# Kernel optimization log

Hardware: AMD Instinct MI355X
Metric: run time of the kernel (lower is better)

The kernel has to match this reference:

```python
import jax, jax.numpy as jnp
import numpy as np

N_CH = 256          # EEG channels = graph nodes
T = 100000          # timesteps
CNN_OUT = 32
GRU_H = 64
GNN_H = 32
N_CLS = 2
THRESH = 0.7


def _conv1d(x, w, b, stride, pad):
    # x: [N, C_in, L], w: [C_out, C_in, K]
    y = jax.lax.conv_general_dilated(
        x, w, window_strides=(stride,), padding=[(pad, pad)],
        dimension_numbers=("NCH", "OIH", "NCH"))
    return y + b[None, :, None]


def _gru_last_hidden(xs, wih, whh, bih, bhh):
    # xs: [S, N, in], returns final hidden [N, H] (PyTorch GRU equations)
    H = whh.shape[1]
    h0 = jnp.zeros((xs.shape[1], H), xs.dtype)

    def step(h, x):
        gi = x @ wih.T + bih          # [N, 3H]
        gh = h @ whh.T + bhh
        i_r, i_z, i_n = jnp.split(gi, 3, axis=-1)
        h_r, h_z, h_n = jnp.split(gh, 3, axis=-1)
        r = jax.nn.sigmoid(i_r + h_r)
        z = jax.nn.sigmoid(i_z + h_z)
        n = jnp.tanh(i_n + r * h_n)
        h = (1.0 - z) * n + z * h
        return h, None

    hT, _ = jax.lax.scan(step, h0, xs)
    return hT


def _pairwise_corrcoef(x):
    x = x - x.mean(axis=1, keepdims=True)
    x = x / (x.std(axis=1, keepdims=True, ddof=1) + 1e-6)  # torch std is unbiased
    return (x @ x.T) / x.shape[1]


def _gcn(x, A_hat, w, b):
    # PyG GCNConv: A_hat @ (x @ W^T) + b  (sym-normalized adj w/ self-loops)
    return A_hat @ (x @ w.T) + b


def setup_inputs() -> dict:
    key = jax.random.key(0)
    ks = jax.random.split(key, 24)
    r = lambda i, shape, s: (jax.random.normal(ks[i], shape, jnp.float32) * s)
    d = {
        "data": r(0, (N_CH, T), 1.0),
        "conv1_w": r(1, (8, 1, 11), 0.3), "conv1_b": r(2, (8,), 0.1),
        "conv2_w": r(3, (16, 8, 7), 0.1), "conv2_b": r(4, (16,), 0.1),
        "conv3_w": r(5, (CNN_OUT, 16, 5), 0.1), "conv3_b": r(6, (CNN_OUT,), 0.1),
        "gru_wih_f": r(7, (3 * GRU_H, CNN_OUT), 0.1), "gru_whh_f": r(8, (3 * GRU_H, GRU_H), 0.1),
        "gru_bih_f": r(9, (3 * GRU_H,), 0.05), "gru_bhh_f": r(10, (3 * GRU_H,), 0.05),
        "gru_wih_b": r(11, (3 * GRU_H, CNN_OUT), 0.1), "gru_whh_b": r(12, (3 * GRU_H, GRU_H), 0.1),
        "gru_bih_b": r(13, (3 * GRU_H,), 0.05), "gru_bhh_b": r(14, (3 * GRU_H,), 0.05),
        "gcn1_w": r(15, (GNN_H, 2 * GRU_H), 0.1), "gcn1_b": r(16, (GNN_H,), 0.05),
        "gcn2_w": r(17, (GNN_H, GNN_H), 0.15), "gcn2_b": r(18, (GNN_H,), 0.05),
        "cls_w": r(19, (N_CLS, GNN_H), 0.15), "cls_b": r(20, (N_CLS,), 0.05),
    }
    return d


def reference(data, conv1_w, conv1_b, conv2_w, conv2_b, conv3_w, conv3_b,
              gru_wih_f, gru_whh_f, gru_bih_f, gru_bhh_f,
              gru_wih_b, gru_whh_b, gru_bih_b, gru_bhh_b,
              gcn1_w, gcn1_b, gcn2_w, gcn2_b, cls_w, cls_b):
    x = data[:, None, :]                                 # [N, 1, T]
    x = jax.nn.relu(_conv1d(x, conv1_w, conv1_b, 5, 5))  # [N, 8, 20000]
    x = jax.nn.relu(_conv1d(x, conv2_w, conv2_b, 5, 3))  # [N, 16, 4000]
    x = jax.nn.relu(_conv1d(x, conv3_w, conv3_b, 5, 2))  # [N, 32, 800]
    xs = jnp.transpose(x, (2, 0, 1))                     # [S=800, N, 32]

    h_f = _gru_last_hidden(xs, gru_wih_f, gru_whh_f, gru_bih_f, gru_bhh_f)
    h_b = _gru_last_hidden(xs[::-1], gru_wih_b, gru_whh_b, gru_bih_b, gru_bhh_b)
    # torch h_n.permute(1,0,2).reshape(N,-1) -> concat [fwd, bwd]
    h_n = jnp.concatenate([h_f, h_b], axis=-1)           # [N, 128]

    corr = _pairwise_corrcoef(h_n)                       # [N, N]
    # dense adjacency = thresholded |corr|; diagonal is ~1 so self-loops present
    # (matches PyG add_remaining_self_loops: already there). Always nonempty.
    A = (jnp.abs(corr) > THRESH).astype(h_n.dtype)
    deg = A.sum(axis=1)
    dinv = jax.lax.rsqrt(jnp.maximum(deg, 1e-12))
    A_hat = A * dinv[:, None] * dinv[None, :]            # D^-1/2 A D^-1/2

    h = jax.nn.relu(_gcn(h_n, A_hat, gcn1_w, gcn1_b))
    h = jax.nn.relu(_gcn(h, A_hat, gcn2_w, gcn2_b))
    graph_emb = h.mean(axis=0, keepdims=True)            # [1, GNN_H]
    return graph_emb @ cls_w.T + cls_b                   # [1, N_CLS]
```

## Files before the change

### kernel.cpp

```cpp
#include <hip/hip_runtime.h>
#include <math.h>

#define N_CH 256
#define T_IN 100000
#define L1O 20000
#define L2O 4000
#define L3O 800
#define C1 8
#define C2 16
#define C3 32

#define TILE3 25
#define NY2   125
#define NY1   627
#define ND    3141

__device__ __forceinline__ float sigm(float x) {
    x = fminf(fmaxf(x, -30.0f), 30.0f);
    return 1.0f / (1.0f + __expf(-x));
}
__device__ __forceinline__ float tanhfast(float x) {
    x = fminf(fmaxf(x, -15.0f), 15.0f);
    float e = __expf(-2.0f * x);
    return (1.0f - e) / (1.0f + e);
}
__device__ __forceinline__ float bcast(float v, int lane) {
    return __int_as_float(__builtin_amdgcn_readlane(__float_as_int(v), lane));
}
__device__ __forceinline__ float f4e(const float4& v, int e) {
    return ((const float*)&v)[e];
}

__global__ __launch_bounds__(256) void k_conv(
    const float* __restrict__ data,
    const float* __restrict__ w1, const float* __restrict__ b1,
    const float* __restrict__ w2, const float* __restrict__ b2,
    const float* __restrict__ w3, const float* __restrict__ b3,
    float* __restrict__ x3)
{
    __shared__ __align__(16) float sd[ND];
    __shared__ __align__(16) float sy1[NY1][C1];
    __shared__ __align__(16) float sy2[NY2][C2];

    const int tid = threadIdx.x;
    const int tb  = blockIdx.x;
    const int ch  = blockIdx.y;
    const int t0    = tb * TILE3;
    const int dbase = 3125 * tb - 70;
    const int ubase = 625 * tb - 13;
    const int sbase = 125 * tb - 2;

    const float* dch = data + (size_t)ch * T_IN;
    for (int e = tid; e < ND; e += 256) {
        int g = dbase + e;
        sd[e] = (g >= 0 && g < T_IN) ? dch[g] : 0.0f;
    }
    __syncthreads();

    for (int u = tid; u < NY1; u += 256) {
        int ug = ubase + u;
        bool ok = (ug >= 0 && ug < L1O);
        float t[11];
        #pragma unroll
        for (int k = 0; k < 11; ++k) t[k] = sd[5 * u + k];
        float acc[8];
        #pragma unroll
        for (int c = 0; c < 8; ++c) acc[c] = b1[c];
        #pragma unroll
        for (int k = 0; k < 11; ++k) {
            float tv = t[k];
            #pragma unroll
            for (int c = 0; c < 8; ++c) acc[c] = fmaf(w1[c * 11 + k], tv, acc[c]);
        }
        float4 o0, o1;
        o0.x = ok ? fmaxf(acc[0], 0.f) : 0.f;  o0.y = ok ? fmaxf(acc[1], 0.f) : 0.f;
        o0.z = ok ? fmaxf(acc[2], 0.f) : 0.f;  o0.w = ok ? fmaxf(acc[3], 0.f) : 0.f;
        o1.x = ok ? fmaxf(acc[4], 0.f) : 0.f;  o1.y = ok ? fmaxf(acc[5], 0.f) : 0.f;
        o1.z = ok ? fmaxf(acc[6], 0.f) : 0.f;  o1.w = ok ? fmaxf(acc[7], 0.f) : 0.f;
        ((float4*)&sy1[u][0])[0] = o0;
        ((float4*)&sy1[u][0])[1] = o1;
    }
    __syncthreads();

    {
        const int s    = tid & 127;
        const int half = tid >> 7;
        if (s < NY2) {
            int sg = sbase + s;
            bool ok = (sg >= 0 && sg < L2O);
            float tp[56];
            #pragma unroll
            for (int k = 0; k < 7; ++k) {
                float4 a = ((const float4*)&sy1[5 * s + k][0])[0];
                float4 b = ((const float4*)&sy1[5 * s + k][0])[1];
                tp[k * 8 + 0] = a.x; tp[k * 8 + 1] = a.y; tp[k * 8 + 2] = a.z; tp[k * 8 + 3] = a.w;
                tp[k * 8 + 4] = b.x; tp[k * 8 + 5] = b.y; tp[k * 8 + 6] = b.z; tp[k * 8 + 7] = b.w;
            }
            const int c0 = half * 8;
            float acc[8];
            #pragma unroll
            for (int cc = 0; cc < 8; ++cc) acc[cc] = b2[c0 + cc];
            #pragma unroll
            for (int cc = 0; cc < 8; ++cc) {
                const float* wp = w2 + (c0 + cc) * 56;
                float a = acc[cc];
                #pragma unroll
                for (int ci = 0; ci < 8; ++ci)
                    #pragma unroll
                    for (int k = 0; k < 7; ++k)
                        a = fmaf(wp[ci * 7 + k], tp[k * 8 + ci], a);
                acc[cc] = a;
            }
            float4 o0, o1;
            o0.x = ok ? fmaxf(acc[0], 0.f) : 0.f;  o0.y = ok ? fmaxf(acc[1], 0.f) : 0.f;
            o0.z = ok ? fmaxf(acc[2], 0.f) : 0.f;  o0.w = ok ? fmaxf(acc[3], 0.f) : 0.f;
            o1.x = ok ? fmaxf(acc[4], 0.f) : 0.f;  o1.y = ok ? fmaxf(acc[5], 0.f) : 0.f;
            o1.z = ok ? fmaxf(acc[6], 0.f) : 0.f;  o1.w = ok ? fmaxf(acc[7], 0.f) : 0.f;
            ((float4*)&sy2[s][c0])[0] = o0;
            ((float4*)&sy2[s][c0])[1] = o1;
        }
    }
    __syncthreads();

    {
        const int s    = tid & 127;
        const int half = tid >> 7;
        if (s < TILE3) {
            float tp[80];
            #pragma unroll
            for (int k = 0; k < 5; ++k) {
                #pragma unroll
                for (int q = 0; q < 4; ++q) {
                    float4 a = ((const float4*)&sy2[5 * s + k][0])[q];
                    tp[k * 16 + q * 4 + 0] = a.x; tp[k * 16 + q * 4 + 1] = a.y;
                    tp[k * 16 + q * 4 + 2] = a.z; tp[k * 16 + q * 4 + 3] = a.w;
                }
            }
            const int o0 = half * 16;
            float* xo = x3 + ((size_t)ch * L3O + (t0 + s)) * C3 + o0;
            #pragma unroll
            for (int oo = 0; oo < 16; ++oo) {
                const float* wp = w3 + (o0 + oo) * 80;
                float a = b3[o0 + oo];
                #pragma unroll
                for (int ci = 0; ci < 16; ++ci)
                    #pragma unroll
                    for (int k = 0; k < 5; ++k)
                        a = fmaf(wp[ci * 5 + k], tp[k * 16 + ci], a);
                xo[oo] = fmaxf(a, 0.f);
            }
        }
    }
}

__global__ __launch_bounds__(256) void k_gru5(
    const float* __restrict__ x3,
    const float* __restrict__ wih_f, const float* __restrict__ bih_f,
    const float* __restrict__ whh_f, const float* __restrict__ bhh_f,
    const float* __restrict__ wih_b, const float* __restrict__ bih_b,
    const float* __restrict__ whh_b, const float* __restrict__ bhh_b,
    float* __restrict__ hN)
{
    const int tid = threadIdx.x;
    const int l   = tid & 63;
    const int w   = tid >> 6;
    const int ch = blockIdx.x, dir = blockIdx.y;
    const float* wih = dir ? wih_b : wih_f;
    const float* whh = dir ? whh_b : whh_f;
    const float* bih = dir ? bih_b : bih_f;
    const float* bhh = dir ? bhh_b : bhh_f;

    __shared__ float sdot[2][4][4][64];

    float4 whq[12];
    #pragma unroll
    for (int g = 0; g < 3; ++g)
        #pragma unroll
        for (int q = 0; q < 4; ++q)
            whq[g * 4 + q] = *(const float4*)&whh[(g * 64 + l) * 64 + w * 16 + q * 4];
    float4 wiq[6];
    #pragma unroll
    for (int g = 0; g < 3; ++g)
        #pragma unroll
        for (int q = 0; q < 2; ++q)
            wiq[g * 2 + q] = *(const float4*)&wih[(g * 64 + l) * 32 + w * 8 + q * 4];

    const float br   = bih[l] + bhh[l];
    const float bz   = bih[64 + l] + bhh[64 + l];
    const float bin_ = bih[128 + l];
    const float bhn  = bhh[128 + l];

    const float* xp = x3 + (size_t)ch * L3O * 32 + (l & 31);
    const int xstride = dir ? -32 : 32;
    if (dir) xp += (size_t)(L3O - 1) * 32;
    float x0 = xp[0]; xp += xstride;
    float x1 = xp[0]; xp += xstride;
    float x2 = xp[0]; xp += xstride;

    float h = 0.0f;
    const int kb = w * 16;
    const int xb = w * 8;

    for (int s = 0; s < L3O; ++s) {
        float xn_ = 0.0f;
        if (s + 3 < L3O) xn_ = xp[0];
        xp += xstride;

        float pr = 0.f, pz = 0.f, pn = 0.f;
        #pragma unroll
        for (int q = 0; q < 4; ++q)
            #pragma unroll
            for (int e = 0; e < 4; ++e) {
                float hb = bcast(h, kb + q * 4 + e);
                pr = fmaf(f4e(whq[q],     e), hb, pr);
                pz = fmaf(f4e(whq[4 + q], e), hb, pz);
                pn = fmaf(f4e(whq[8 + q], e), hb, pn);
            }
        float ir = 0.f, iz = 0.f, in_ = 0.f;
        #pragma unroll
        for (int q = 0; q < 2; ++q)
            #pragma unroll
            for (int e = 0; e < 4; ++e) {
                float xv = bcast(x0, xb + q * 4 + e);
                ir  = fmaf(f4e(wiq[q],     e), xv, ir);
                iz  = fmaf(f4e(wiq[2 + q], e), xv, iz);
                in_ = fmaf(f4e(wiq[4 + q], e), xv, in_);
            }

        const int p = s & 1;
        sdot[p][w][0][l] = pr + ir;
        sdot[p][w][1][l] = pz + iz;
        sdot[p][w][2][l] = pn;
        sdot[p][w][3][l] = in_;
        __syncthreads();

        float sr = br, sz_ = bz, snh = bhn, sni = bin_;
        #pragma unroll
        for (int ww = 0; ww < 4; ++ww) {
            sr  += sdot[p][ww][0][l];
            sz_ += sdot[p][ww][1][l];
            snh += sdot[p][ww][2][l];
            sni += sdot[p][ww][3][l];
        }
        float r = sigm(sr);
        float z = sigm(sz_);
        float n = tanhfast(sni + r * snh);
        h = (1.0f - z) * n + z * h;

        x0 = x1; x1 = x2; x2 = xn_;
    }
    if (w == 0) hN[ch * 128 + dir * 64 + l] = h;
}

__global__ __launch_bounds__(128) void k_norm(
    const float* __restrict__ hN, const float* __restrict__ gcn1_w,
    float* __restrict__ Xn, float* __restrict__ XnT, float* __restrict__ hw1)
{
    const int i = blockIdx.x, tid = threadIdx.x;
    __shared__ float red[128];
    __shared__ float row[128];
    float v = hN[i * 128 + tid];
    row[tid] = v;
    red[tid] = v;
    __syncthreads();
    for (int s = 64; s > 0; s >>= 1) { if (tid < s) red[tid] += red[tid + s]; __syncthreads(); }
    float mean = red[0] / 128.0f;
    __syncthreads();
    float d = v - mean;
    red[tid] = d * d;
    __syncthreads();
    for (int s = 64; s > 0; s >>= 1) { if (tid < s) red[tid] += red[tid + s]; __syncthreads(); }
    float sd = sqrtf(red[0] / 127.0f);
    float xn = d / (sd + 1e-6f);
    Xn[i * 128 + tid] = xn;
    XnT[tid * 256 + i] = xn;
    if (tid < 32) {
        float acc = 0.f;
        for (int k = 0; k < 128; ++k) acc += row[k] * gcn1_w[tid * 128 + k];
        hw1[i * 32 + tid] = acc;
    }
}

__global__ __launch_bounds__(256) void k_corr(
    const float* __restrict__ Xn, const float* __restrict__ XnT,
    float* __restrict__ A, float* __restrict__ deg)
{
    const int i = blockIdx.x, tid = threadIdx.x;
    __shared__ float xi[128];
    __shared__ float red[256];
    if (tid < 128) xi[tid] = Xn[i * 128 + tid];
    __syncthreads();
    float c = 0.f;
    for (int k = 0; k < 128; ++k) c += xi[k] * XnT[k * 256 + tid];
    c *= (1.0f / 128.0f);
    float a = (fabsf(c) > 0.7f) ? 1.0f : 0.0f;
    A[i * 256 + tid] = a;
    red[tid] = a;
    __syncthreads();
    for (int s = 128; s > 0; s >>= 1) { if (tid < s) red[tid] += red[tid + s]; __syncthreads(); }
    if (tid == 0) deg[i] = red[0];
}

__global__ __launch_bounds__(256) void k_gcn(
    const float* __restrict__ A, const float* __restrict__ deg,
    const float* __restrict__ hw, const float* __restrict__ bias,
    const float* __restrict__ wNext,
    float* __restrict__ hOut, float* __restrict__ hwNext)
{
    const int i = blockIdx.x, tid = threadIdx.x;
    const int f = tid & 31, grp = tid >> 5;
    __shared__ float aj[256];
    __shared__ float red[8][32];
    __shared__ float hrow[32];
    float dj = rsqrtf(fmaxf(deg[tid], 1e-12f));
    aj[tid] = A[i * 256 + tid] * dj;
    __syncthreads();
    float p = 0.f;
    for (int j = grp * 32; j < grp * 32 + 32; ++j) p += aj[j] * hw[j * 32 + f];
    red[grp][f] = p;
    __syncthreads();
    if (grp == 0) {
        float s = 0.f;
        #pragma unroll
        for (int g = 0; g < 8; ++g) s += red[g][f];
        float di = rsqrtf(fmaxf(deg[i], 1e-12f));
        float o = fmaxf(bias[f] + di * s, 0.0f);
        hOut[i * 32 + f] = o;
        hrow[f] = o;
    }
    __syncthreads();
    if (wNext != nullptr && grp == 0) {
        float acc = 0.f;
        #pragma unroll
        for (int k = 0; k < 32; ++k) acc += hrow[k] * wNext[f * 32 + k];
        hwNext[i * 32 + f] = acc;
    }
}

__global__ __launch_bounds__(64) void k_head(
    const float* __restrict__ h2, const float* __restrict__ cls_w,
    const float* __restrict__ cls_b, float* __restrict__ out)
{
    const int tid = threadIdx.x;
    __shared__ float mean[32];
    if (tid < 32) {
        float s = 0.f;
        for (int i = 0; i < 256; ++i) s += h2[i * 32 + tid];
        mean[tid] = s * (1.0f / 256.0f);
    }
    __syncthreads();
    if (tid < 2) {
        float s = cls_b[tid];
        #pragma unroll
        for (int fe = 0; fe < 32; ++fe) s += mean[fe] * cls_w[tid * 32 + fe];
        out[tid] = s;
    }
}

extern "C" void kernel_launch(void* const* d_in, const int* in_sizes, int n_in,
                              void* d_out, int out_size, void* d_ws, size_t ws_size,
                              hipStream_t stream) {
    const float* data    = (const float*)d_in[0];
    const float* conv1_w = (const float*)d_in[1];
    const float* conv1_b = (const float*)d_in[2];
    const float* conv2_w = (const float*)d_in[3];
    const float* conv2_b = (const float*)d_in[4];
    const float* conv3_w = (const float*)d_in[5];
    const float* conv3_b = (const float*)d_in[6];
    const float* wih_f   = (const float*)d_in[7];
    const float* whh_f   = (const float*)d_in[8];
    const float* bih_f   = (const float*)d_in[9];
    const float* bhh_f   = (const float*)d_in[10];
    const float* wih_b   = (const float*)d_in[11];
    const float* whh_b   = (const float*)d_in[12];
    const float* bih_b   = (const float*)d_in[13];
    const float* bhh_b   = (const float*)d_in[14];
    const float* gcn1_w  = (const float*)d_in[15];
    const float* gcn1_b  = (const float*)d_in[16];
    const float* gcn2_w  = (const float*)d_in[17];
    const float* gcn2_b  = (const float*)d_in[18];
    const float* cls_w   = (const float*)d_in[19];
    const float* cls_b   = (const float*)d_in[20];

    float* ws  = (float*)d_ws;
    float* x3  = ws;
    float* hN  = x3 + 6553600;
    float* Xn  = hN + 32768;
    float* XnT = Xn + 32768;
    float* A   = XnT + 32768;
    float* deg = A + 65536;
    float* hw1 = deg + 256;
    float* h1  = hw1 + 8192;
    float* hw2 = h1 + 8192;
    float* h2  = hw2 + 8192;

    k_conv<<<dim3(32, 256), 256, 0, stream>>>(data, conv1_w, conv1_b, conv2_w, conv2_b,
                                              conv3_w, conv3_b, x3);
    k_gru5<<<dim3(256, 2), 256, 0, stream>>>(x3, wih_f, bih_f, whh_f, bhh_f,
                                             wih_b, bih_b, whh_b, bhh_b, hN);
    k_norm<<<256, 128, 0, stream>>>(hN, gcn1_w, Xn, XnT, hw1);
    k_corr<<<256, 256, 0, stream>>>(Xn, XnT, A, deg);
    k_gcn<<<256, 256, 0, stream>>>(A, deg, hw1, gcn1_b, gcn2_w, h1, hw2);
    k_gcn<<<256, 256, 0, stream>>>(A, deg, hw2, gcn2_b, nullptr, h2, nullptr);
    k_head<<<1, 64, 0, stream>>>(h2, cls_w, cls_b, (float*)d_out);
}
```

Measured before the change: 1.093 ms.

## Restructure GRU kernel to one gate per wave with full-row register weights

The GRU recurrence kernel now uses 3 waves (192 threads), one per gate. Each lane holds a full 64-element hidden-weight row and a 32-element input-weight row in registers, so it computes complete dot products without the former 4-wave split-K partial sums. This removes the cross-wave reduction from shared memory and issues fewer LDS writes per step. It also adds multiple accumulators for ILP and a waves_per_eu(1,1) attribute to allow high register use. In exchange each lane's serial dot-product chain is longer and occupancy is lower.

Measured after the change: 1.538 ms. 40.7% more time.

```diff
diff --git a/kernel.cpp b/kernel.cpp
--- a/kernel.cpp
+++ b/kernel.cpp
@@ -26,9 +26,6 @@
 }
 __device__ __forceinline__ float bcast(float v, int lane) {
     return __int_as_float(__builtin_amdgcn_readlane(__float_as_int(v), lane));
-}
-__device__ __forceinline__ float f4e(const float4& v, int e) {
-    return ((const float*)&v)[e];
 }
 
 __global__ __launch_bounds__(256) void k_conv(
@@ -153,7 +150,8 @@
     }
 }
 
-__global__ __launch_bounds__(256) void k_gru5(
+__global__ __attribute__((amdgpu_waves_per_eu(1, 1))) __launch_bounds__(192)
+void k_gru6(
     const float* __restrict__ x3,
     const float* __restrict__ wih_f, const float* __restrict__ bih_f,
     const float* __restrict__ whh_f, const float* __restrict__ bhh_f,
@@ -161,95 +159,93 @@
     const float* __restrict__ whh_b, const float* __restrict__ bhh_b,
     float* __restrict__ hN)
 {
-    const int tid = threadIdx.x;
-    const int l   = tid & 63;
-    const int w   = tid >> 6;
+    const int tid  = threadIdx.x;
+    const int lane = tid & 63;
+    const int g    = tid >> 6;
     const int ch = blockIdx.x, dir = blockIdx.y;
     const float* wih = dir ? wih_b : wih_f;
     const float* whh = dir ? whh_b : whh_f;
     const float* bih = dir ? bih_b : bih_f;
     const float* bhh = dir ? bhh_b : bhh_f;
-
-    __shared__ float sdot[2][4][4][64];
-
-    float4 whq[12];
-    #pragma unroll
-    for (int g = 0; g < 3; ++g)
-        #pragma unroll
-        for (int q = 0; q < 4; ++q)
-            whq[g * 4 + q] = *(const float4*)&whh[(g * 64 + l) * 64 + w * 16 + q * 4];
-    float4 wiq[6];
-    #pragma unroll
-    for (int g = 0; g < 3; ++g)
-        #pragma unroll
-        for (int q = 0; q < 2; ++q)
-            wiq[g * 2 + q] = *(const float4*)&wih[(g * 64 + l) * 32 + w * 8 + q * 4];
-
-    const float br   = bih[l] + bhh[l];
-    const float bz   = bih[64 + l] + bhh[64 + l];
-    const float bin_ = bih[128 + l];
-    const float bhn  = bhh[128 + l];
-
-    const float* xp = x3 + (size_t)ch * L3O * 32 + (l & 31);
+    const int row = g * 64 + lane;
+
+    __shared__ float sdot[2][4][64];
+
+    float w[64];
+    {
+        const float4* w4 = (const float4*)(whh + row * 64);
+        #pragma unroll
+        for (int q = 0; q < 16; ++q) {
+            float4 v = w4[q];
+            w[4*q] = v.x; w[4*q+1] = v.y; w[4*q+2] = v.z; w[4*q+3] = v.w;
+        }
+    }
+    float wi[32];
+    {
+        const float4* w4 = (const float4*)(wih + row * 32);
+        #pragma unroll
+        for (int q = 0; q < 8; ++q) {
+            float4 v = w4[q];
+            wi[4*q] = v.x; wi[4*q+1] = v.y; wi[4*q+2] = v.z; wi[4*q+3] = v.w;
+        }
+    }
+
+    const float bi = bih[row];
+    const float bh = bhh[row];
+
+    const float* xp = x3 + (size_t)ch * L3O * 32 + (lane & 31);
     const int xstride = dir ? -32 : 32;
     if (dir) xp += (size_t)(L3O - 1) * 32;
+
     float x0 = xp[0]; xp += xstride;
     float x1 = xp[0]; xp += xstride;
     float x2 = xp[0]; xp += xstride;
 
     float h = 0.0f;
-    const int kb = w * 16;
-    const int xb = w * 8;
 
     for (int s = 0; s < L3O; ++s) {
-        float xn_ = 0.0f;
-        if (s + 3 < L3O) xn_ = xp[0];
+        float xnext = 0.0f;
+        if (s + 3 < L3O) xnext = xp[0];
         xp += xstride;
 
-        float pr = 0.f, pz = 0.f, pn = 0.f;
-        #pragma unroll
-        for (int q = 0; q < 4; ++q)
-            #pragma unroll
-            for (int e = 0; e < 4; ++e) {
-                float hb = bcast(h, kb + q * 4 + e);
-                pr = fmaf(f4e(whq[q],     e), hb, pr);
-                pz = fmaf(f4e(whq[4 + q], e), hb, pz);
-                pn = fmaf(f4e(whq[8 + q], e), hb, pn);
-            }
-        float ir = 0.f, iz = 0.f, in_ = 0.f;
-        #pragma unroll
-        for (int q = 0; q < 2; ++q)
-            #pragma unroll
-            for (int e = 0; e < 4; ++e) {
-                float xv = bcast(x0, xb + q * 4 + e);
-                ir  = fmaf(f4e(wiq[q],     e), xv, ir);
-                iz  = fmaf(f4e(wiq[2 + q], e), xv, iz);
-                in_ = fmaf(f4e(wiq[4 + q], e), xv, in_);
-            }
+        float a0 = bi, a0b = 0.0f;
+        #pragma unroll
+        for (int k = 0; k < 32; k += 2) {
+            a0  = fmaf(wi[k],     bcast(x0, k),     a0);
+            a0b = fmaf(wi[k + 1], bcast(x0, k + 1), a0b);
+        }
+        float a1 = bh, a1b = 0.0f, a1c = 0.0f, a1d = 0.0f;
+        #pragma unroll
+        for (int j = 0; j < 64; j += 4) {
+            a1  = fmaf(w[j],     bcast(h, j),     a1);
+            a1b = fmaf(w[j + 1], bcast(h, j + 1), a1b);
+            a1c = fmaf(w[j + 2], bcast(h, j + 2), a1c);
+            a1d = fmaf(w[j + 3], bcast(h, j + 3), a1d);
+        }
+        float ai = a0 + a0b;
+        float ah = (a1 + a1b) + (a1c + a1d);
 
         const int p = s & 1;
-        sdot[p][w][0][l] = pr + ir;
-        sdot[p][w][1][l] = pz + iz;
-        sdot[p][w][2][l] = pn;
-        sdot[p][w][3][l] = in_;
+        if (g < 2) {
+            sdot[p][g][lane] = ai + ah;
+        } else {
+            sdot[p][2][lane] = ah;
+            sdot[p][3][lane] = ai;
+        }
         __syncthreads();
 
-        float sr = br, sz_ = bz, snh = bhn, sni = bin_;
-        #pragma unroll
-        for (int ww = 0; ww < 4; ++ww) {
-            sr  += sdot[p][ww][0][l];
-            sz_ += sdot[p][ww][1][l];
-            snh += sdot[p][ww][2][l];
-            sni += sdot[p][ww][3][l];
-        }
+        float sr  = sdot[p][0][lane];
+        float sz  = sdot[p][1][lane];
+        float shn = sdot[p][2][lane];
+        float sin_= sdot[p][3][lane];
         float r = sigm(sr);
-        float z = sigm(sz_);
-        float n = tanhfast(sni + r * snh);
+        float z = sigm(sz);
+        float n = tanhfast(sin_ + r * shn);
         h = (1.0f - z) * n + z * h;
 
-        x0 = x1; x1 = x2; x2 = xn_;
-    }
-    if (w == 0) hN[ch * 128 + dir * 64 + l] = h;
+        x0 = x1; x1 = x2; x2 = xnext;
+    }
+    if (g == 0) hN[ch * 128 + dir * 64 + lane] = h;
 }
 
 __global__ __launch_bounds__(128) void k_norm(
@@ -396,7 +392,7 @@
 
     k_conv<<<dim3(32, 256), 256, 0, stream>>>(data, conv1_w, conv1_b, conv2_w, conv2_b,
                                               conv3_w, conv3_b, x3);
-    k_gru5<<<dim3(256, 2), 256, 0, stream>>>(x3, wih_f, bih_f, whh_f, bhh_f,
+    k_gru6<<<dim3(256, 2), 192, 0, stream>>>(x3, wih_f, bih_f, whh_f, bhh_f,
                                              wih_b, bih_b, whh_b, bhh_b, hN);
     k_norm<<<256, 128, 0, stream>>>(hN, gcn1_w, Xn, XnT, hw1);
     k_corr<<<256, 256, 0, stream>>>(Xn, XnT, A, deg);
```
